# Kernel tuning notes

Hardware: AMD Instinct MI355X
Metric: run time of the kernel (lower is better)

The kernel has to match this reference:

```python
import jax, jax.numpy as jnp
import numpy as np

TEMPERATURE = 8.0  # sqrt(head_dim=64)
NEG_INF = -1.0e9


def setup_inputs() -> dict:
    key = jax.random.key(0)
    kq, kk, kv, ks, km = jax.random.split(key, 5)
    B, H, S, D = 4, 8, 1024, 64
    q = jax.random.normal(kq, (B, H, S, D), dtype=jnp.float32)
    k = jax.random.normal(kk, (B, H, S, D), dtype=jnp.float32)
    v = jax.random.normal(kv, (B, H, S, D), dtype=jnp.float32)
    sph = jax.random.uniform(ks, (B, H, S, S), dtype=jnp.float32)
    mask = jax.random.randint(km, (B, 1, S, S), 0, 2, dtype=jnp.int32)
    return {"q": q, "k": k, "v": v, "sph": sph, "mask": mask}


def reference(q, k, v, sph, mask):
    # scores: [B,H,S,S]
    attn = jnp.einsum("bhqd,bhkd->bhqk", q / TEMPERATURE, k)
    attn = attn * sph
    attn = jnp.where(mask == 0, NEG_INF, attn)
    p_attn = jax.nn.softmax(attn, axis=-1)  # dropout in eval mode = identity
    output = jnp.einsum("bhqk,bhkd->bhqd", p_attn, v)
    return (output, p_attn)
```

## Files before the change

### kernel.cpp

```cpp
#include <hip/hip_runtime.h>

#define S_DIM 1024
#define TQ 16
#define LOG2E 1.44269504f

typedef __attribute__((ext_vector_type(4))) float f32x4;
typedef __attribute__((ext_vector_type(4))) int i32x4;
typedef _Float16 half4 __attribute__((ext_vector_type(4)));
typedef _Float16 half8 __attribute__((ext_vector_type(8)));

__device__ inline half8 pack8h(f32x4 a, f32x4 b) {
  half8 r;
  r[0] = (_Float16)a.x; r[1] = (_Float16)a.y;
  r[2] = (_Float16)a.z; r[3] = (_Float16)a.w;
  r[4] = (_Float16)b.x; r[5] = (_Float16)b.y;
  r[6] = (_Float16)b.z; r[7] = (_Float16)b.w;
  return r;
}

__global__ __launch_bounds__(256)
void prep_kernel(const float* __restrict__ kp, const float* __restrict__ vp,
                 _Float16* __restrict__ k16, _Float16* __restrict__ vt16)
{
  __shared__ _Float16 tile[64][72];
  const int tid = threadIdx.x;
  const int bh  = blockIdx.x >> 4;
  const int c0  = (blockIdx.x & 15) * 64;
  const size_t base = ((size_t)bh * S_DIM + c0) * 64;

  #pragma unroll
  for (int i = 0; i < 4; ++i) {
    const int idx = i * 256 + tid;
    f32x4 kv = *(const f32x4*)(kp + base + (size_t)idx * 4);
    half4 h; h[0] = (_Float16)kv.x; h[1] = (_Float16)kv.y;
    h[2] = (_Float16)kv.z; h[3] = (_Float16)kv.w;
    *(half4*)(k16 + base + (size_t)idx * 4) = h;
  }
  #pragma unroll
  for (int i = 0; i < 4; ++i) {
    const int idx = i * 256 + tid;
    const int r = idx >> 4, c4 = idx & 15;
    f32x4 vv = *(const f32x4*)(vp + base + (size_t)r * 64 + c4 * 4);
    tile[c4 * 4 + 0][r] = (_Float16)vv.x;
    tile[c4 * 4 + 1][r] = (_Float16)vv.y;
    tile[c4 * 4 + 2][r] = (_Float16)vv.z;
    tile[c4 * 4 + 3][r] = (_Float16)vv.w;
  }
  __syncthreads();
  #pragma unroll
  for (int i = 0; i < 2; ++i) {
    const int idx = i * 256 + tid;
    const int d = idx >> 3, g = idx & 7;
    half8 h = *(half8*)&tile[d][g * 8];
    *(half8*)(vt16 + ((size_t)bh * 64 + d) * S_DIM + c0 + g * 8) = h;
  }
}

__global__ __launch_bounds__(256)
void maskpack_kernel(const int* __restrict__ maskp, unsigned int* __restrict__ pm)
{
  const int tid  = threadIdx.x;
  const int lane = tid & 63;
  const int wave = tid >> 6;
  const int row  = blockIdx.x;
  const size_t base = (size_t)row * S_DIM + wave * 256;
  unsigned long long bal0, bal1, bal2, bal3;
  bal0 = __ballot(maskp[base +   0 + lane] != 0);
  bal1 = __ballot(maskp[base +  64 + lane] != 0);
  bal2 = __ballot(maskp[base + 128 + lane] != 0);
  bal3 = __ballot(maskp[base + 192 + lane] != 0);
  if (lane == 0) {
    unsigned long long* dst =
        (unsigned long long*)(pm + (size_t)row * 32 + wave * 8);
    dst[0] = bal0; dst[1] = bal1; dst[2] = bal2; dst[3] = bal3;
  }
}

__global__ __launch_bounds__(256, 4)
void sdpa_kernel(const float* __restrict__ qp,
                 const _Float16* __restrict__ k16,
                 const _Float16* __restrict__ vt16,
                 const float* __restrict__ sphp,
                 const unsigned int* __restrict__ pm,
                 float* __restrict__ outp, float* __restrict__ pp)
{
  __shared__ _Float16 pb[TQ][1032];
  __shared__ float    red[4][16];

  const int tid   = threadIdx.x;
  const int lane  = tid & 63;
  const int wave  = tid >> 6;
  const int row16 = lane & 15;
  const int quad  = lane >> 4;

  const int bh = blockIdx.x >> 6;
  const int qt = blockIdx.x & 63;
  const int b  = bh >> 3;
  const int q0 = qt * TQ;
  const size_t bhS = (size_t)bh * S_DIM;

  const int kb = wave * 256;
  const int ll = lane & 31;
  const int lh = lane >> 5;
  const int kcol2 = kb + ll * 8;

  const unsigned int* pmbase = pm + ((size_t)b * S_DIM + q0) * 32 + wave * 8 + (ll >> 2);
  unsigned int mb[8];
  #pragma unroll
  for (int i = 0; i < 8; ++i) mb[i] = pmbase[(size_t)(2 * i + lh) * 32];
  const int msh = (ll & 3) * 8;

  f32x4 sA[4][2], sB[4][2];
  #pragma unroll
  for (int i = 0; i < 4; ++i) {
    const float* p = sphp + (bhS + q0 + 2 * i + lh) * S_DIM + kcol2;
    sA[i][0] = __builtin_nontemporal_load((const f32x4*)p);
    sA[i][1] = __builtin_nontemporal_load((const f32x4*)(p + 4));
  }

  const float* qrow = qp + (bhS + q0 + row16) * 64 + quad * 8;
  const f32x4 s8 = {0.125f, 0.125f, 0.125f, 0.125f};
  f32x4 qa = *(const f32x4*)(qrow);
  f32x4 qb = *(const f32x4*)(qrow + 4);
  f32x4 qc = *(const f32x4*)(qrow + 32);
  f32x4 qd = *(const f32x4*)(qrow + 36);
  const half8 bq0 = pack8h(qa * s8, qb * s8);
  const half8 bq1 = pack8h(qc * s8, qd * s8);

  const _Float16* kbp = k16 + (bhS + kb) * 64;
  #pragma unroll
  for (int t = 0; t < 16; ++t) {
    const _Float16* krow = kbp + (t * 16 + row16) * 64 + quad * 8;
    half8 a0 = *(const half8*)(krow);
    half8 a1 = *(const half8*)(krow + 32);
    f32x4 acc = {0.f, 0.f, 0.f, 0.f};
    acc = __builtin_amdgcn_mfma_f32_16x16x32_f16(a0, bq0, acc, 0, 0, 0);
    acc = __builtin_amdgcn_mfma_f32_16x16x32_f16(a1, bq1, acc, 0, 0, 0);
    half4 hv;
    hv[0] = (_Float16)(acc.x * LOG2E); hv[1] = (_Float16)(acc.y * LOG2E);
    hv[2] = (_Float16)(acc.z * LOG2E); hv[3] = (_Float16)(acc.w * LOG2E);
    *(half4*)&pb[row16][kb + t * 16 + quad * 4] = hv;
  }

  auto proc = [&](int i, const f32x4* sv, unsigned int mbi) {
    const int r = 2 * i + lh;
    half8 sh = *(half8*)&pb[r][kcol2];
    const unsigned int m = (mbi >> msh) & 0xFFu;
    float x0 = (float)sh[0] * sv[0].x, x1 = (float)sh[1] * sv[0].y;
    float x2 = (float)sh[2] * sv[0].z, x3 = (float)sh[3] * sv[0].w;
    float x4 = (float)sh[4] * sv[1].x, x5 = (float)sh[5] * sv[1].y;
    float x6 = (float)sh[6] * sv[1].z, x7 = (float)sh[7] * sv[1].w;
    float e0 = (m &   1u) ? __builtin_amdgcn_exp2f(x0) : 0.f;
    float e1 = (m &   2u) ? __builtin_amdgcn_exp2f(x1) : 0.f;
    float e2 = (m &   4u) ? __builtin_amdgcn_exp2f(x2) : 0.f;
    float e3 = (m &   8u) ? __builtin_amdgcn_exp2f(x3) : 0.f;
    float e4 = (m &  16u) ? __builtin_amdgcn_exp2f(x4) : 0.f;
    float e5 = (m &  32u) ? __builtin_amdgcn_exp2f(x5) : 0.f;
    float e6 = (m &  64u) ? __builtin_amdgcn_exp2f(x6) : 0.f;
    float e7 = (m & 128u) ? __builtin_amdgcn_exp2f(x7) : 0.f;
    half8 hv;
    hv[0] = (_Float16)e0; hv[1] = (_Float16)e1;
    hv[2] = (_Float16)e2; hv[3] = (_Float16)e3;
    hv[4] = (_Float16)e4; hv[5] = (_Float16)e5;
    hv[6] = (_Float16)e6; hv[7] = (_Float16)e7;
    *(half8*)&pb[r][kcol2] = hv;
    float sum = ((e0 + e1) + (e2 + e3)) + ((e4 + e5) + (e6 + e7));
    #pragma unroll
    for (int off = 16; off > 0; off >>= 1)
      sum += __shfl_xor(sum, off);
    if (ll == 0) red[wave][r] = sum;
  };

  #pragma unroll
  for (int i = 0; i < 4; ++i) {
    const float* p = sphp + (bhS + q0 + 8 + 2 * i + lh) * S_DIM + kcol2;
    sB[i][0] = __builtin_nontemporal_load((const f32x4*)p);
    sB[i][1] = __builtin_nontemporal_load((const f32x4*)(p + 4));
  }
  #pragma unroll
  for (int i = 0; i < 4; ++i) proc(i, sA[i], mb[i]);
  #pragma unroll
  for (int i = 0; i < 4; ++i) proc(4 + i, sB[i], mb[4 + i]);

  __syncthreads();

  #pragma unroll
  for (int i = 0; i < 8; ++i) {
    const int r = 2 * i + lh;
    const float inv = __builtin_amdgcn_rcpf(
        (red[0][r] + red[1][r]) + (red[2][r] + red[3][r]));
    half8 e = *(half8*)&pb[r][kcol2];
    f32x4 p0, p1;
    p0.x = (float)e[0] * inv; p0.y = (float)e[1] * inv;
    p0.z = (float)e[2] * inv; p0.w = (float)e[3] * inv;
    p1.x = (float)e[4] * inv; p1.y = (float)e[5] * inv;
    p1.z = (float)e[6] * inv; p1.w = (float)e[7] * inv;
    float* dst = pp + (bhS + q0 + r) * S_DIM + kcol2;
    __builtin_nontemporal_store(p0, (f32x4*)dst);
    __builtin_nontemporal_store(p1, (f32x4*)(dst + 4));
  }

  f32x4 oacc = {0.f, 0.f, 0.f, 0.f};
  const _Float16* vrow = vt16 + ((size_t)bh * 64 + wave * 16 + row16) * S_DIM + quad * 8;
  #pragma unroll 8
  for (int c = 0; c < 32; ++c) {
    half8 af = *(const half8*)(vrow + c * 32);
    half8 bf = *(const half8*)&pb[row16][c * 32 + quad * 8];
    oacc = __builtin_amdgcn_mfma_f32_16x16x32_f16(af, bf, oacc, 0, 0, 0);
  }

  const float ssum = (red[0][row16] + red[1][row16]) + (red[2][row16] + red[3][row16]);
  const float invq = __builtin_amdgcn_rcpf(ssum);
  float* orow = outp + (bhS + q0 + row16) * 64 + wave * 16 + quad * 4;
  *(f32x4*)orow = oacc * invq;
}

extern "C" void kernel_launch(void* const* d_in, const int* in_sizes, int n_in,
                              void* d_out, int out_size, void* d_ws, size_t ws_size,
                              hipStream_t stream) {
  const float* q    = (const float*)d_in[0];
  const float* k    = (const float*)d_in[1];
  const float* v    = (const float*)d_in[2];
  const float* sph  = (const float*)d_in[3];
  const int*   mask = (const int*)d_in[4];
  float* out  = (float*)d_out;
  float* patt = out + (size_t)4 * 8 * 1024 * 64;

  _Float16* k16  = (_Float16*)d_ws;
  _Float16* vt16 = k16 + (size_t)32 * S_DIM * 64;
  unsigned int* pm = (unsigned int*)(vt16 + (size_t)32 * S_DIM * 64);

  hipLaunchKernelGGL(maskpack_kernel, dim3(4 * S_DIM), dim3(256), 0, stream,
                     mask, pm);
  hipLaunchKernelGGL(prep_kernel, dim3(32 * 16), dim3(256), 0, stream,
                     k, v, k16, vt16);
  hipLaunchKernelGGL(sdpa_kernel, dim3(32 * 64), dim3(256), 0, stream,
                     q, k16, vt16, sph, pm, out, patt);
}
```

Before: 320.6 us.

## Fuse score, sph scaling and exp into MFMA loop with async sph prefetch

Restructures the score phase so the sph tile is fetched per 16-column step via global_load_lds into a 4-deep LDS ring, with K fragments prefetched three steps ahead. Exp, masking and row-sum accumulation happen right on the MFMA accumulator, so the fp16 round trip of raw scores through LDS and the separate elementwise pass go away. LOG2E is folded into the Q scale. The extra 16 KB of staging LDS lowers the occupancy hint from 4 to 3 blocks per CU, and the hand-written waitcnt counts must match the number of outstanding loads.

```diff
diff --git a/kernel.cpp b/kernel.cpp
--- a/kernel.cpp
+++ b/kernel.cpp
@@ -2,20 +2,25 @@
 
 #define S_DIM 1024
 #define TQ 16
-#define LOG2E 1.44269504f
+#define QS 0.180336880f
 
 typedef __attribute__((ext_vector_type(4))) float f32x4;
-typedef __attribute__((ext_vector_type(4))) int i32x4;
 typedef _Float16 half4 __attribute__((ext_vector_type(4)));
 typedef _Float16 half8 __attribute__((ext_vector_type(8)));
 
-__device__ inline half8 pack8h(f32x4 a, f32x4 b) {
+__device__ __forceinline__ half8 pack8h(f32x4 a, f32x4 b) {
   half8 r;
   r[0] = (_Float16)a.x; r[1] = (_Float16)a.y;
   r[2] = (_Float16)a.z; r[3] = (_Float16)a.w;
   r[4] = (_Float16)b.x; r[5] = (_Float16)b.y;
   r[6] = (_Float16)b.z; r[7] = (_Float16)b.w;
   return r;
+}
+
+__device__ __forceinline__ void dma16(const float* gsrc, float* ldst) {
+  __builtin_amdgcn_global_load_lds(
+      (const __attribute__((address_space(1))) unsigned int*)gsrc,
+      (__attribute__((address_space(3))) unsigned int*)ldst, 16, 0, 0);
 }
 
 __global__ __launch_bounds__(256)
@@ -76,7 +81,7 @@
   }
 }
 
-__global__ __launch_bounds__(256, 4)
+__global__ __launch_bounds__(256, 3)
 void sdpa_kernel(const float* __restrict__ qp,
                  const _Float16* __restrict__ k16,
                  const _Float16* __restrict__ vt16,
@@ -85,7 +90,8 @@
                  float* __restrict__ outp, float* __restrict__ pp)
 {
   __shared__ _Float16 pb[TQ][1032];
-  __shared__ float    red[4][16];
+  __shared__ float    sstage[4][4][256];
+  __shared__ float    red[4][TQ];
 
   const int tid   = threadIdx.x;
   const int lane  = tid & 63;
@@ -98,92 +104,73 @@
   const int b  = bh >> 3;
   const int q0 = qt * TQ;
   const size_t bhS = (size_t)bh * S_DIM;
-
   const int kb = wave * 256;
-  const int ll = lane & 31;
-  const int lh = lane >> 5;
-  const int kcol2 = kb + ll * 8;
-
-  const unsigned int* pmbase = pm + ((size_t)b * S_DIM + q0) * 32 + wave * 8 + (ll >> 2);
+
+  const unsigned int* pmrow = pm + ((size_t)b * S_DIM + q0 + row16) * 32 + wave * 8;
   unsigned int mb[8];
   #pragma unroll
-  for (int i = 0; i < 8; ++i) mb[i] = pmbase[(size_t)(2 * i + lh) * 32];
-  const int msh = (ll & 3) * 8;
-
-  f32x4 sA[4][2], sB[4][2];
-  #pragma unroll
-  for (int i = 0; i < 4; ++i) {
-    const float* p = sphp + (bhS + q0 + 2 * i + lh) * S_DIM + kcol2;
-    sA[i][0] = __builtin_nontemporal_load((const f32x4*)p);
-    sA[i][1] = __builtin_nontemporal_load((const f32x4*)(p + 4));
-  }
+  for (int i = 0; i < 8; ++i) mb[i] = pmrow[i];
 
   const float* qrow = qp + (bhS + q0 + row16) * 64 + quad * 8;
-  const f32x4 s8 = {0.125f, 0.125f, 0.125f, 0.125f};
+  const f32x4 qs = {QS, QS, QS, QS};
   f32x4 qa = *(const f32x4*)(qrow);
   f32x4 qb = *(const f32x4*)(qrow + 4);
   f32x4 qc = *(const f32x4*)(qrow + 32);
   f32x4 qd = *(const f32x4*)(qrow + 36);
-  const half8 bq0 = pack8h(qa * s8, qb * s8);
-  const half8 bq1 = pack8h(qc * s8, qd * s8);
+  const half8 bq0 = pack8h(qa * qs, qb * qs);
+  const half8 bq1 = pack8h(qc * qs, qd * qs);
 
   const _Float16* kbp = k16 + (bhS + kb) * 64;
-  #pragma unroll
-  for (int t = 0; t < 16; ++t) {
-    const _Float16* krow = kbp + (t * 16 + row16) * 64 + quad * 8;
-    half8 a0 = *(const half8*)(krow);
-    half8 a1 = *(const half8*)(krow + 32);
-    f32x4 acc = {0.f, 0.f, 0.f, 0.f};
-    acc = __builtin_amdgcn_mfma_f32_16x16x32_f16(a0, bq0, acc, 0, 0, 0);
-    acc = __builtin_amdgcn_mfma_f32_16x16x32_f16(a1, bq1, acc, 0, 0, 0);
-    half4 hv;
-    hv[0] = (_Float16)(acc.x * LOG2E); hv[1] = (_Float16)(acc.y * LOG2E);
-    hv[2] = (_Float16)(acc.z * LOG2E); hv[3] = (_Float16)(acc.w * LOG2E);
-    *(half4*)&pb[row16][kb + t * 16 + quad * 4] = hv;
-  }
-
-  auto proc = [&](int i, const f32x4* sv, unsigned int mbi) {
-    const int r = 2 * i + lh;
-    half8 sh = *(half8*)&pb[r][kcol2];
-    const unsigned int m = (mbi >> msh) & 0xFFu;
-    float x0 = (float)sh[0] * sv[0].x, x1 = (float)sh[1] * sv[0].y;
-    float x2 = (float)sh[2] * sv[0].z, x3 = (float)sh[3] * sv[0].w;
-    float x4 = (float)sh[4] * sv[1].x, x5 = (float)sh[5] * sv[1].y;
-    float x6 = (float)sh[6] * sv[1].z, x7 = (float)sh[7] * sv[1].w;
-    float e0 = (m &   1u) ? __builtin_amdgcn_exp2f(x0) : 0.f;
-    float e1 = (m &   2u) ? __builtin_amdgcn_exp2f(x1) : 0.f;
-    float e2 = (m &   4u) ? __builtin_amdgcn_exp2f(x2) : 0.f;
-    float e3 = (m &   8u) ? __builtin_amdgcn_exp2f(x3) : 0.f;
-    float e4 = (m &  16u) ? __builtin_amdgcn_exp2f(x4) : 0.f;
-    float e5 = (m &  32u) ? __builtin_amdgcn_exp2f(x5) : 0.f;
-    float e6 = (m &  64u) ? __builtin_amdgcn_exp2f(x6) : 0.f;
-    float e7 = (m & 128u) ? __builtin_amdgcn_exp2f(x7) : 0.f;
-    half8 hv;
-    hv[0] = (_Float16)e0; hv[1] = (_Float16)e1;
-    hv[2] = (_Float16)e2; hv[3] = (_Float16)e3;
-    hv[4] = (_Float16)e4; hv[5] = (_Float16)e5;
-    hv[6] = (_Float16)e6; hv[7] = (_Float16)e7;
-    *(half8*)&pb[r][kcol2] = hv;
-    float sum = ((e0 + e1) + (e2 + e3)) + ((e4 + e5) + (e6 + e7));
-    #pragma unroll
-    for (int off = 16; off > 0; off >>= 1)
-      sum += __shfl_xor(sum, off);
-    if (ll == 0) red[wave][r] = sum;
-  };
-
-  #pragma unroll
-  for (int i = 0; i < 4; ++i) {
-    const float* p = sphp + (bhS + q0 + 8 + 2 * i + lh) * S_DIM + kcol2;
-    sB[i][0] = __builtin_nontemporal_load((const f32x4*)p);
-    sB[i][1] = __builtin_nontemporal_load((const f32x4*)(p + 4));
-  }
-  #pragma unroll
-  for (int i = 0; i < 4; ++i) proc(i, sA[i], mb[i]);
-  #pragma unroll
-  for (int i = 0; i < 4; ++i) proc(4 + i, sB[i], mb[4 + i]);
+  const float* sph_lane = sphp + (bhS + q0 + row16) * S_DIM + kb + quad * 4;
+
+  half8 kA0[4], kA1[4];
+  float lanesum = 0.f;
+
+  #define PREF(T) do {                                                        \
+    dma16(sph_lane + (T) * 16, &sstage[wave][(T) & 3][0]);                    \
+    const _Float16* krow_ = kbp + ((T) * 16 + row16) * 64 + quad * 8;         \
+    kA0[(T) & 3] = *(const half8*)(krow_);                                    \
+    kA1[(T) & 3] = *(const half8*)(krow_ + 32);                               \
+  } while (0)
+
+  #define STEP(T, WN) do {                                                    \
+    if ((T) + 3 < 16) { PREF((T) + 3); }                                      \
+    asm volatile("s_waitcnt vmcnt(" #WN ") lgkmcnt(0)" ::: "memory");         \
+    f32x4 s4 = *(const f32x4*)&sstage[wave][(T) & 3][lane * 4];               \
+    f32x4 acc = {0.f, 0.f, 0.f, 0.f};                                         \
+    acc = __builtin_amdgcn_mfma_f32_16x16x32_f16(kA0[(T) & 3], bq0, acc, 0, 0, 0); \
+    acc = __builtin_amdgcn_mfma_f32_16x16x32_f16(kA1[(T) & 3], bq1, acc, 0, 0, 0); \
+    const unsigned int m4 = (mb[(T) >> 1] >> (((T) & 1) * 16 + quad * 4)) & 0xFu; \
+    float e0 = (m4 & 1u) ? __builtin_amdgcn_exp2f(acc.x * s4.x) : 0.f;        \
+    float e1 = (m4 & 2u) ? __builtin_amdgcn_exp2f(acc.y * s4.y) : 0.f;        \
+    float e2 = (m4 & 4u) ? __builtin_amdgcn_exp2f(acc.z * s4.z) : 0.f;        \
+    float e3 = (m4 & 8u) ? __builtin_amdgcn_exp2f(acc.w * s4.w) : 0.f;        \
+    half4 hv; hv[0] = (_Float16)e0; hv[1] = (_Float16)e1;                     \
+    hv[2] = (_Float16)e2; hv[3] = (_Float16)e3;                               \
+    *(half4*)&pb[row16][kb + (T) * 16 + quad * 4] = hv;                       \
+    lanesum += (e0 + e1) + (e2 + e3);                                         \
+  } while (0)
+
+  PREF(0); asm volatile("" ::: "memory");
+  PREF(1); asm volatile("" ::: "memory");
+  PREF(2); asm volatile("" ::: "memory");
+
+  STEP( 0, 9); STEP( 1, 9); STEP( 2, 9); STEP( 3, 9);
+  STEP( 4, 9); STEP( 5, 9); STEP( 6, 9); STEP( 7, 9);
+  STEP( 8, 9); STEP( 9, 9); STEP(10, 9); STEP(11, 9);
+  STEP(12, 9); STEP(13, 6); STEP(14, 3); STEP(15, 0);
+  #undef STEP
+  #undef PREF
+
+  lanesum += __shfl_xor(lanesum, 16);
+  lanesum += __shfl_xor(lanesum, 32);
+  if (lane < 16) red[wave][lane] = lanesum;
 
   __syncthreads();
 
+  const int ll = lane & 31;
+  const int lh = lane >> 5;
+  const int kcol2 = kb + ll * 8;
   #pragma unroll
   for (int i = 0; i < 8; ++i) {
     const int r = 2 * i + lh;
```

Result: no change. 321.8 us (+0.4%).
